# Kernel tuning notes

Measured on AMD Instinct MI355X. Metric: run time of the kernel, lower is better.

The kernel has to match this reference:

```python
import jax, jax.numpy as jnp
import numpy as np

D_MODEL = 1024
N_HEADS = 16
D_KV = D_MODEL // N_HEADS
MAX_SEQ = 2048
THETA = 10000.0
BATCH = 2
SEQ = 2048


def setup_inputs() -> dict:
    key = jax.random.key(0)
    ks = jax.random.split(key, 5)
    std = np.sqrt(2.0 / (D_MODEL + D_MODEL))
    x = jax.random.normal(ks[0], (BATCH, SEQ, D_MODEL), dtype=jnp.float32)
    wq = jax.random.normal(ks[1], (D_MODEL, D_MODEL), dtype=jnp.float32) * std
    wk = jax.random.normal(ks[2], (D_MODEL, D_MODEL), dtype=jnp.float32) * std
    wv = jax.random.normal(ks[3], (D_MODEL, D_MODEL), dtype=jnp.float32) * std
    wo = jax.random.normal(ks[4], (D_MODEL, D_MODEL), dtype=jnp.float32) * std
    token_positions = jnp.arange(SEQ, dtype=jnp.int32)
    return {"x": x, "wq": wq, "wk": wk, "wv": wv, "wo": wo,
            "token_positions": token_positions}


def _rope_tables():
    freq_range = jnp.arange(D_KV // 2, dtype=jnp.float32)
    freq = 1.0 / (THETA ** (2.0 * freq_range / D_KV))
    pos = jnp.arange(MAX_SEQ, dtype=jnp.float32)
    angs = pos[:, None] * freq[None, :]  # [max_seq, d_kv/2]
    return jnp.cos(angs), jnp.sin(angs)


def _apply_rope(xh, token_positions, cos_t, sin_t):
    # xh: [b, h, s, d_kv]
    cos_f = jnp.repeat(cos_t[token_positions], 2, axis=-1)  # [s, d_kv]
    sin_f = jnp.repeat(sin_t[token_positions], 2, axis=-1)
    pairs = xh.reshape(*xh.shape[:-1], D_KV // 2, 2)
    even, odd = pairs[..., 0], pairs[..., 1]
    rot = jnp.stack([-odd, even], axis=-1).reshape(xh.shape)
    return xh * cos_f + rot * sin_f


def reference(x, wq, wk, wv, wo, token_positions):
    b, s, _ = x.shape
    def heads(y):
        return y.reshape(b, s, N_HEADS, D_KV).transpose(0, 2, 1, 3)  # [b,h,s,d]
    q = heads(jnp.einsum('bsi,oi->bso', x, wq))
    k = heads(jnp.einsum('bsi,oi->bso', x, wk))
    v = heads(jnp.einsum('bsi,oi->bso', x, wv))
    cos_t, sin_t = _rope_tables()
    q = _apply_rope(q, token_positions, cos_t, sin_t)
    k = _apply_rope(k, token_positions, cos_t, sin_t)
    scale = 1.0 / jnp.sqrt(jnp.asarray(D_KV, x.dtype))
    scores = jnp.einsum('bhqd,bhkd->bhqk', q, k) * scale
    causal = jnp.tril(jnp.ones((s, s), dtype=bool))
    scores = jnp.where(causal, scores, -jnp.inf)
    probs = jax.nn.softmax(scores, axis=-1)
    attn = jnp.einsum('bhqk,bhkd->bhqd', probs, v)
    attn = attn.transpose(0, 2, 1, 3).reshape(b, s, D_MODEL)
    return jnp.einsum('bsi,oi->bso', attn, wo)
```

## Files before the change

kernel.cpp:

```cpp
#include <hip/hip_runtime.h>
#include <hip/hip_bf16.h>
#include <math.h>

#define SEQ 2048
#define DM 1024
#define NH 16
#define DKV 64
#define MTOT 4096
#define PSTR 40

typedef __attribute__((ext_vector_type(8))) short bf16x8;
typedef __attribute__((ext_vector_type(4))) short s16x4;
typedef __attribute__((ext_vector_type(4))) float f32x4;
typedef unsigned short ushort_t;

__device__ __forceinline__ short f2bf(float f) {
    union { float f; unsigned u; } v; v.f = f;
    unsigned r = v.u + 0x7fffu + ((v.u >> 16) & 1u);
    return (short)(r >> 16);
}

__device__ __forceinline__ bf16x8 cvt8(f32x4 a, f32x4 b) {
    union { __hip_bfloat162 h[4]; bf16x8 v; } u;
    u.h[0] = __float22bfloat162_rn(float2{a[0], a[1]});
    u.h[1] = __float22bfloat162_rn(float2{a[2], a[3]});
    u.h[2] = __float22bfloat162_rn(float2{b[0], b[1]});
    u.h[3] = __float22bfloat162_rn(float2{b[2], b[3]});
    return u.v;
}

__device__ __forceinline__ s16x4 cvt4(float a, float b, float c, float d) {
    union { __hip_bfloat162 h[2]; s16x4 v; } u;
    u.h[0] = __float22bfloat162_rn(float2{a, b});
    u.h[1] = __float22bfloat162_rn(float2{c, d});
    return u.v;
}

__device__ __forceinline__ void gload_lds16(const void* g, void* l) {
    __builtin_amdgcn_global_load_lds(
        (const __attribute__((address_space(1))) unsigned int*)g,
        (__attribute__((address_space(3))) unsigned int*)l, 16, 0, 0);
}

__global__ void cvt_kernel(const float* __restrict__ wq, const float* __restrict__ wk,
                           const float* __restrict__ wv, ushort_t* __restrict__ Wqkv) {
    int tid = blockIdx.x * blockDim.x + threadIdx.x;
    int z = tid >> 17;
    int off = (tid & 131071) * 8;
    const float* src = (z == 0) ? wq : (z == 1) ? wk : wv;
    f32x4 a = ((const f32x4*)(src + off))[0];
    f32x4 b = ((const f32x4*)(src + off))[1];
    *(bf16x8*)&Wqkv[(size_t)z * 1048576 + off] = cvt8(a, b);
}

__global__ void cvt_x_kernel(const float* __restrict__ x, ushort_t* __restrict__ xb) {
    int tid = blockIdx.x * blockDim.x + threadIdx.x;
    int off = tid * 8;
    f32x4 a = ((const f32x4*)(x + off))[0];
    f32x4 b = ((const f32x4*)(x + off))[1];
    *(bf16x8*)&xb[off] = cvt8(a, b);
}

__global__ void rope_table_kernel(float* __restrict__ cos_t, float* __restrict__ sin_t) {
    int tid = blockIdx.x * blockDim.x + threadIdx.x;
    int i = tid & 31, pos = tid >> 5;
    double freq = pow(10000.0, -(double)(2 * i) / 64.0);
    double ang = (double)pos * freq;
    cos_t[tid] = (float)cos(ang);
    sin_t[tid] = (float)sin(ang);
}

__global__ __launch_bounds__(256) void proj_qkv_kernel(
    const ushort_t* __restrict__ xb, const ushort_t* __restrict__ Wqkv,
    const float* __restrict__ cos_t, const float* __restrict__ sin_t,
    const int* __restrict__ tokpos,
    ushort_t* __restrict__ Qg, ushort_t* __restrict__ Kg, ushort_t* __restrict__ Vt)
{
    __shared__ __align__(16) short lA[2][128 * 32];
    __shared__ __align__(16) short lB[2][128 * 32];

    const int t = threadIdx.x;
    const int lane = t & 63;
    const int wid = t >> 6;
    const int quad = lane >> 4, l16 = lane & 15;
    const int mh = wid >> 1, nh = wid & 1;
    const int Mb = blockIdx.y * 128;
    const int NbG = blockIdx.x * 128;
    const int z = NbG >> 10;
    const int Nb = NbG & 1023;

    f32x4 acc[4][4] = {};

    auto stage = [&](int buf, int k0) {
        #pragma unroll
        for (int i = 0; i < 2; ++i) {
            int rbase = wid * 32 + i * 16;
            int row = rbase + (lane >> 2);
            int gch = (lane & 3) ^ ((lane >> 3) & 3);
            gload_lds16(xb + (size_t)(Mb + row) * DM + k0 + gch * 8, &lA[buf][rbase * 32]);
        }
        #pragma unroll
        for (int i = 0; i < 2; ++i) {
            int rbase = wid * 32 + i * 16;
            int row = rbase + (lane >> 2);
            int gch = (lane & 3) ^ ((lane >> 3) & 3);
            gload_lds16(Wqkv + (size_t)(NbG + row) * DM + k0 + gch * 8, &lB[buf][rbase * 32]);
        }
    };

    stage(0, 0);

    for (int kt = 0; kt < 32; ++kt) {
        const int cur = kt & 1;
        __syncthreads();
        if (kt < 31) stage(cur ^ 1, kt * 32 + 32);

        bf16x8 a[4], b[4];
        #pragma unroll
        for (int mt = 0; mt < 4; ++mt) {
            int row = mh * 64 + mt * 16 + l16;
            int slot = quad ^ ((l16 >> 1) & 3);
            a[mt] = *(const bf16x8*)&lA[cur][row * 32 + slot * 8];
        }
        #pragma unroll
        for (int nt = 0; nt < 4; ++nt) {
            int row = nh * 64 + nt * 16 + l16;
            int slot = quad ^ ((l16 >> 1) & 3);
            b[nt] = *(const bf16x8*)&lB[cur][row * 32 + slot * 8];
        }
        #pragma unroll
        for (int mt = 0; mt < 4; ++mt)
            #pragma unroll
            for (int nt = 0; nt < 4; ++nt)
                acc[mt][nt] = __builtin_amdgcn_mfma_f32_16x16x32_bf16(a[mt], b[nt], acc[mt][nt], 0, 0, 0);
    }

    const int bb = Mb >> 11;
    if (z == 2) {
        #pragma unroll
        for (int mt = 0; mt < 4; ++mt) {
            const int s0 = (Mb + mh * 64 + mt * 16 + quad * 4) & (SEQ - 1);
            #pragma unroll
            for (int nt = 0; nt < 4; ++nt) {
                int col = Nb + nh * 64 + nt * 16 + l16;
                int h = col >> 6, d = col & 63;
                s16x4 pk;
                #pragma unroll
                for (int r = 0; r < 4; ++r) pk[r] = f2bf(acc[mt][nt][r]);
                *(s16x4*)&Vt[((size_t)(bb * NH + h) * DKV + d) * SEQ + s0] = pk;
            }
        }
    } else {
        ushort_t* dst = (z == 0) ? Qg : Kg;
        #pragma unroll
        for (int mt = 0; mt < 4; ++mt) {
            #pragma unroll
            for (int nt = 0; nt < 4; ++nt) {
                #pragma unroll
                for (int r = 0; r < 4; ++r) {
                    int row = Mb + mh * 64 + mt * 16 + quad * 4 + r;
                    int s = row & (SEQ - 1);
                    int col = Nb + nh * 64 + nt * 16 + l16;
                    int h = col >> 6, d = col & 63;
                    float val = acc[mt][nt][r];
                    float part = __shfl_xor(val, 1, 64);
                    int pos = tokpos[s];
                    int i = d >> 1;
                    float c = cos_t[pos * 32 + i];
                    float sn = sin_t[pos * 32 + i];
                    val = (d & 1) ? (val * c + part * sn) : (val * c - part * sn);
                    dst[((size_t)(bb * NH + h) * SEQ + s) * DKV + d] = (ushort_t)f2bf(val);
                }
            }
        }
    }
}

__global__ __launch_bounds__(128, 4) void attn_kernel(
    const ushort_t* __restrict__ Q, const ushort_t* __restrict__ K,
    const ushort_t* __restrict__ Vt, ushort_t* __restrict__ O)
{
    __shared__ __align__(16) short lK[2][32 * 64];
    __shared__ __align__(16) short lV[2][64 * 32];
    __shared__ __align__(16) short lP[2][32 * PSTR];

    const int t = threadIdx.x;
    const int lane = t & 63;
    const int wid = t >> 6;
    const int quad = lane >> 4, l16 = lane & 15;
    const int bh = blockIdx.y;
    const int qt = gridDim.x - 1 - blockIdx.x;
    const int q0 = qt * 64;
    const int q0w = q0 + wid * 32;
    const int nkt = 2 * qt + 2;

    const ushort_t* Qb = Q + (size_t)bh * SEQ * DKV;
    const ushort_t* Kb = K + (size_t)bh * SEQ * DKV;
    const ushort_t* Vtb = Vt + (size_t)bh * DKV * SEQ;

    auto stage = [&](int kb, int buf) {
        #pragma unroll
        for (int j = 0; j < 2; ++j) {
            int rbase = wid * 16 + j * 8;
            int row = rbase + (lane >> 3);
            int gch = (lane & 7) ^ (row & 7);
            gload_lds16(Kb + (size_t)(kb + row) * DKV + gch * 8, &lK[buf][rbase * 64]);
        }
        #pragma unroll
        for (int j = 0; j < 2; ++j) {
            int rbase = wid * 32 + j * 16;
            int row = rbase + (lane >> 2);
            int gch = (lane & 3) ^ ((lane >> 3) & 3);
            gload_lds16(Vtb + (size_t)row * SEQ + kb + gch * 8, &lV[buf][rbase * 32]);
        }
    };

    bf16x8 bq[2][2];
    #pragma unroll
    for (int nt = 0; nt < 2; ++nt)
        #pragma unroll
        for (int h = 0; h < 2; ++h)
            bq[nt][h] = *(const bf16x8*)(Qb + (size_t)(q0w + nt * 16 + l16) * DKV + h * 32 + quad * 8);

    f32x4 acc[2][4] = {};
    float ps[2] = {0.f, 0.f};
    short* myP = lP[wid];

    stage(0, 0);

    for (int kt = 0; kt < nkt; ++kt) {
        const int kbase = kt * 32;
        __syncthreads();
        if (kt + 1 < nkt) stage(kbase + 32, (kt + 1) & 1);

        const short* bK = lK[kt & 1];
        const short* bV = lV[kt & 1];

        bf16x8 ak[2][2];
        #pragma unroll
        for (int mt = 0; mt < 2; ++mt)
            #pragma unroll
            for (int h = 0; h < 2; ++h) {
                int row = mt * 16 + l16;
                int slot = (h * 4 + quad) ^ (row & 7);
                ak[mt][h] = *(const bf16x8*)&bK[row * 64 + slot * 8];
            }

        f32x4 st[2][2];
        #pragma unroll
        for (int mt = 0; mt < 2; ++mt)
            #pragma unroll
            for (int nt = 0; nt < 2; ++nt) {
                f32x4 zz = {};
                zz = __builtin_amdgcn_mfma_f32_16x16x32_bf16(ak[mt][0], bq[nt][0], zz, 0, 0, 0);
                zz = __builtin_amdgcn_mfma_f32_16x16x32_bf16(ak[mt][1], bq[nt][1], zz, 0, 0, 0);
                st[mt][nt] = zz;
            }

        if (kbase >= q0w) {
            #pragma unroll
            for (int mt = 0; mt < 2; ++mt)
                #pragma unroll
                for (int nt = 0; nt < 2; ++nt) {
                    float pv[4];
                    #pragma unroll
                    for (int r = 0; r < 4; ++r) {
                        int k_abs = kbase + mt * 16 + quad * 4 + r;
                        int q_abs = q0w + nt * 16 + l16;
                        pv[r] = (k_abs > q_abs) ? 0.f : __expf(st[mt][nt][r] * 0.125f);
                        ps[nt] += pv[r];
                    }
                    *(s16x4*)&myP[(nt * 16 + l16) * PSTR + mt * 16 + quad * 4] =
                        cvt4(pv[0], pv[1], pv[2], pv[3]);
                }
        } else {
            #pragma unroll
            for (int mt = 0; mt < 2; ++mt)
                #pragma unroll
                for (int nt = 0; nt < 2; ++nt) {
                    float pv[4];
                    #pragma unroll
                    for (int r = 0; r < 4; ++r) {
                        pv[r] = __expf(st[mt][nt][r] * 0.125f);
                        ps[nt] += pv[r];
                    }
                    *(s16x4*)&myP[(nt * 16 + l16) * PSTR + mt * 16 + quad * 4] =
                        cvt4(pv[0], pv[1], pv[2], pv[3]);
                }
        }

        bf16x8 ap[2];
        #pragma unroll
        for (int mg = 0; mg < 2; ++mg)
            ap[mg] = *(const bf16x8*)&myP[(mg * 16 + l16) * PSTR + quad * 8];

        #pragma unroll
        for (int d = 0; d < 4; ++d) {
            int row = d * 16 + l16;
            int slot = quad ^ ((l16 >> 1) & 3);
            bf16x8 bv = *(const bf16x8*)&bV[row * 32 + slot * 8];
            #pragma unroll
            for (int mg = 0; mg < 2; ++mg)
                acc[mg][d] = __builtin_amdgcn_mfma_f32_16x16x32_bf16(ap[mg], bv, acc[mg][d], 0, 0, 0);
        }
    }

    #pragma unroll
    for (int g = 0; g < 2; ++g) {
        float v = ps[g];
        v += __shfl_xor(v, 16, 64);
        v += __shfl_xor(v, 32, 64);
        ps[g] = v;
    }
    float* lLw = (float*)myP;
    if (quad == 0) { lLw[l16] = ps[0]; lLw[16 + l16] = ps[1]; }
    const int bb = bh >> 4, h = bh & 15;
    #pragma unroll
    for (int mg = 0; mg < 2; ++mg) {
        f32x4 lv = *(const f32x4*)&lLw[mg * 16 + quad * 4];
        f32x4 inv;
        #pragma unroll
        for (int r = 0; r < 4; ++r) inv[r] = 1.0f / lv[r];
        #pragma unroll
        for (int d = 0; d < 4; ++d)
            #pragma unroll
            for (int r = 0; r < 4; ++r) {
                int qrow = q0w + mg * 16 + quad * 4 + r;
                int dd = d * 16 + l16;
                O[(size_t)(bb * SEQ + qrow) * DM + h * DKV + dd] = (ushort_t)f2bf(acc[mg][d][r] * inv[r]);
            }
    }
}

__global__ __launch_bounds__(256) void oproj_kernel(
    const ushort_t* __restrict__ A, const float* __restrict__ w, float* __restrict__ out)
{
    __shared__ __align__(16) short lA[2][64 * 32];
    __shared__ __align__(16) float lBf[2][128 * 32];

    const int t = threadIdx.x;
    const int lane = t & 63;
    const int wid = t >> 6;
    const int quad = lane >> 4, l16 = lane & 15;
    const int mh = wid >> 1, nh = wid & 1;
    const int Mb = blockIdx.y * 64;
    const int Nb = blockIdx.x * 128;

    f32x4 acc[2][4] = {};

    auto stage = [&](int buf, int k0) {
        {
            int rbase = wid * 16;
            int row = rbase + (lane >> 2);
            int gch = (lane & 3) ^ ((lane >> 3) & 3);
            gload_lds16(A + (size_t)(Mb + row) * DM + k0 + gch * 8, &lA[buf][rbase * 32]);
        }
        #pragma unroll
        for (int i = 0; i < 4; ++i) {
            int rbase = wid * 32 + i * 8;
            int row = rbase + (lane >> 3);
            int gch = (lane & 7) ^ (row & 7);
            gload_lds16(w + (size_t)(Nb + row) * DM + k0 + gch * 4, &lBf[buf][rbase * 32]);
        }
    };

    stage(0, 0);

    for (int kt = 0; kt < 32; ++kt) {
        const int cur = kt & 1;
        __syncthreads();
        if (kt < 31) stage(cur ^ 1, kt * 32 + 32);

        bf16x8 a[2], b[4];
        #pragma unroll
        for (int mt = 0; mt < 2; ++mt) {
            int row = mh * 32 + mt * 16 + l16;
            int slot = quad ^ ((l16 >> 1) & 3);
            a[mt] = *(const bf16x8*)&lA[cur][row * 32 + slot * 8];
        }
        #pragma unroll
        for (int nt = 0; nt < 4; ++nt) {
            int row = nh * 64 + nt * 16 + l16;
            int p0 = (2 * quad) ^ (row & 7);
            int p1 = (2 * quad + 1) ^ (row & 7);
            f32x4 q0 = *(const f32x4*)&lBf[cur][row * 32 + p0 * 4];
            f32x4 q1 = *(const f32x4*)&lBf[cur][row * 32 + p1 * 4];
            b[nt] = cvt8(q0, q1);
        }
        #pragma unroll
        for (int mt = 0; mt < 2; ++mt)
            #pragma unroll
            for (int nt = 0; nt < 4; ++nt)
                acc[mt][nt] = __builtin_amdgcn_mfma_f32_16x16x32_bf16(a[mt], b[nt], acc[mt][nt], 0, 0, 0);
    }

    #pragma unroll
    for (int mt = 0; mt < 2; ++mt)
        #pragma unroll
        for (int nt = 0; nt < 4; ++nt)
            #pragma unroll
            for (int r = 0; r < 4; ++r) {
                int row = Mb + mh * 32 + mt * 16 + quad * 4 + r;
                int col = Nb + nh * 64 + nt * 16 + l16;
                out[(size_t)row * DM + col] = acc[mt][nt][r];
            }
}

extern "C" void kernel_launch(void* const* d_in, const int* in_sizes, int n_in,
                              void* d_out, int out_size, void* d_ws, size_t ws_size,
                              hipStream_t stream) {
    const float* x  = (const float*)d_in[0];
    const float* wq = (const float*)d_in[1];
    const float* wk = (const float*)d_in[2];
    const float* wv = (const float*)d_in[3];
    const float* wo = (const float*)d_in[4];
    const int* tokpos = (const int*)d_in[5];
    float* out = (float*)d_out;

    char* ws = (char*)d_ws;
    float* cos_t    = (float*)ws;
    float* sin_t    = (float*)(ws + 256 * 1024);
    ushort_t* Wqkv  = (ushort_t*)(ws + 512 * 1024);
    ushort_t* AO    = (ushort_t*)ws;
    ushort_t* Qg    = (ushort_t*)(ws + (size_t)8  * 1024 * 1024);
    ushort_t* Kg    = (ushort_t*)(ws + (size_t)16 * 1024 * 1024);
    ushort_t* Vt    = (ushort_t*)(ws + (size_t)24 * 1024 * 1024);
    ushort_t* xb    = (ushort_t*)d_out;

    cvt_kernel<<<1536, 256, 0, stream>>>(wq, wk, wv, Wqkv);
    cvt_x_kernel<<<2048, 256, 0, stream>>>(x, xb);
    rope_table_kernel<<<256, 256, 0, stream>>>(cos_t, sin_t);
    proj_qkv_kernel<<<dim3(3 * DM / 128, MTOT / 128), 256, 0, stream>>>(
        xb, Wqkv, cos_t, sin_t, tokpos, Qg, Kg, Vt);
    attn_kernel<<<dim3(SEQ / 64, 32), 128, 0, stream>>>(Qg, Kg, Vt, AO);
    oproj_kernel<<<dim3(DM / 128, MTOT / 64), 256, 0, stream>>>(AO, wo, out);
}
```

Baseline: 240.1 us.

## Shrink attention query tile to 32 rows per block with 16 per wave

Each attention block now handles 32 query rows (16 per wave) instead of 64, doubling the grid and raising the occupancy hint to 8 blocks per CU. The causal loop runs qt+1 key tiles per block, and each K/V tile loaded into LDS is reused by half as many query rows. This lowers per-thread registers and improves load balance and parallelism, at the cost of more K/V traffic per query and less MFMA work per LDS load.

```diff
diff --git a/kernel.cpp b/kernel.cpp
--- a/kernel.cpp
+++ b/kernel.cpp
@@ -176,13 +176,13 @@
     }
 }
 
-__global__ __launch_bounds__(128, 4) void attn_kernel(
+__global__ __launch_bounds__(128, 8) void attn_kernel(
     const ushort_t* __restrict__ Q, const ushort_t* __restrict__ K,
     const ushort_t* __restrict__ Vt, ushort_t* __restrict__ O)
 {
     __shared__ __align__(16) short lK[2][32 * 64];
     __shared__ __align__(16) short lV[2][64 * 32];
-    __shared__ __align__(16) short lP[2][32 * PSTR];
+    __shared__ __align__(16) short lP[2][16 * PSTR];
 
     const int t = threadIdx.x;
     const int lane = t & 63;
@@ -190,9 +190,9 @@
     const int quad = lane >> 4, l16 = lane & 15;
     const int bh = blockIdx.y;
     const int qt = gridDim.x - 1 - blockIdx.x;
-    const int q0 = qt * 64;
-    const int q0w = q0 + wid * 32;
-    const int nkt = 2 * qt + 2;
+    const int q0 = qt * 32;
+    const int q0w = q0 + wid * 16;
+    const int nkt = qt + 1;
 
     const ushort_t* Qb = Q + (size_t)bh * SEQ * DKV;
     const ushort_t* Kb = K + (size_t)bh * SEQ * DKV;
@@ -215,15 +215,13 @@
         }
     };
 
-    bf16x8 bq[2][2];
+    bf16x8 bq[2];
     #pragma unroll
-    for (int nt = 0; nt < 2; ++nt)
-        #pragma unroll
-        for (int h = 0; h < 2; ++h)
-            bq[nt][h] = *(const bf16x8*)(Qb + (size_t)(q0w + nt * 16 + l16) * DKV + h * 32 + quad * 8);
-
-    f32x4 acc[2][4] = {};
-    float ps[2] = {0.f, 0.f};
+    for (int h = 0; h < 2; ++h)
+        bq[h] = *(const bf16x8*)(Qb + (size_t)(q0w + l16) * DKV + h * 32 + quad * 8);
+
+    f32x4 acc[4] = {};
+    float ps = 0.f;
     short* myP = lP[wid];
 
     stage(0, 0);
@@ -246,90 +244,69 @@
                 ak[mt][h] = *(const bf16x8*)&bK[row * 64 + slot * 8];
             }
 
-        f32x4 st[2][2];
-        #pragma unroll
-        for (int mt = 0; mt < 2; ++mt)
-            #pragma unroll
-            for (int nt = 0; nt < 2; ++nt) {
-                f32x4 zz = {};
-                zz = __builtin_amdgcn_mfma_f32_16x16x32_bf16(ak[mt][0], bq[nt][0], zz, 0, 0, 0);
-                zz = __builtin_amdgcn_mfma_f32_16x16x32_bf16(ak[mt][1], bq[nt][1], zz, 0, 0, 0);
-                st[mt][nt] = zz;
-            }
-
-        if (kbase >= q0w) {
-            #pragma unroll
-            for (int mt = 0; mt < 2; ++mt)
+        f32x4 st[2];
+        #pragma unroll
+        for (int mt = 0; mt < 2; ++mt) {
+            f32x4 zz = {};
+            zz = __builtin_amdgcn_mfma_f32_16x16x32_bf16(ak[mt][0], bq[0], zz, 0, 0, 0);
+            zz = __builtin_amdgcn_mfma_f32_16x16x32_bf16(ak[mt][1], bq[1], zz, 0, 0, 0);
+            st[mt] = zz;
+        }
+
+        if (kbase + 31 > q0w) {
+            #pragma unroll
+            for (int mt = 0; mt < 2; ++mt) {
+                float pv[4];
                 #pragma unroll
-                for (int nt = 0; nt < 2; ++nt) {
-                    float pv[4];
-                    #pragma unroll
-                    for (int r = 0; r < 4; ++r) {
-                        int k_abs = kbase + mt * 16 + quad * 4 + r;
-                        int q_abs = q0w + nt * 16 + l16;
-                        pv[r] = (k_abs > q_abs) ? 0.f : __expf(st[mt][nt][r] * 0.125f);
-                        ps[nt] += pv[r];
-                    }
-                    *(s16x4*)&myP[(nt * 16 + l16) * PSTR + mt * 16 + quad * 4] =
-                        cvt4(pv[0], pv[1], pv[2], pv[3]);
+                for (int r = 0; r < 4; ++r) {
+                    int k_abs = kbase + mt * 16 + quad * 4 + r;
+                    int q_abs = q0w + l16;
+                    pv[r] = (k_abs > q_abs) ? 0.f : __expf(st[mt][r] * 0.125f);
+                    ps += pv[r];
                 }
+                *(s16x4*)&myP[l16 * PSTR + mt * 16 + quad * 4] = cvt4(pv[0], pv[1], pv[2], pv[3]);
+            }
         } else {
             #pragma unroll
-            for (int mt = 0; mt < 2; ++mt)
+            for (int mt = 0; mt < 2; ++mt) {
+                float pv[4];
                 #pragma unroll
-                for (int nt = 0; nt < 2; ++nt) {
-                    float pv[4];
-                    #pragma unroll
-                    for (int r = 0; r < 4; ++r) {
-                        pv[r] = __expf(st[mt][nt][r] * 0.125f);
-                        ps[nt] += pv[r];
-                    }
-                    *(s16x4*)&myP[(nt * 16 + l16) * PSTR + mt * 16 + quad * 4] =
-                        cvt4(pv[0], pv[1], pv[2], pv[3]);
+                for (int r = 0; r < 4; ++r) {
+                    pv[r] = __expf(st[mt][r] * 0.125f);
+                    ps += pv[r];
                 }
-        }
-
-        bf16x8 ap[2];
-        #pragma unroll
-        for (int mg = 0; mg < 2; ++mg)
-            ap[mg] = *(const bf16x8*)&myP[(mg * 16 + l16) * PSTR + quad * 8];
+                *(s16x4*)&myP[l16 * PSTR + mt * 16 + quad * 4] = cvt4(pv[0], pv[1], pv[2], pv[3]);
+            }
+        }
+
+        bf16x8 ap = *(const bf16x8*)&myP[l16 * PSTR + quad * 8];
 
         #pragma unroll
         for (int d = 0; d < 4; ++d) {
             int row = d * 16 + l16;
             int slot = quad ^ ((l16 >> 1) & 3);
             bf16x8 bv = *(const bf16x8*)&bV[row * 32 + slot * 8];
-            #pragma unroll
-            for (int mg = 0; mg < 2; ++mg)
-                acc[mg][d] = __builtin_amdgcn_mfma_f32_16x16x32_bf16(ap[mg], bv, acc[mg][d], 0, 0, 0);
+            acc[d] = __builtin_amdgcn_mfma_f32_16x16x32_bf16(ap, bv, acc[d], 0, 0, 0);
         }
     }
 
+    ps += __shfl_xor(ps, 16, 64);
+    ps += __shfl_xor(ps, 32, 64);
+    float* lLw = (float*)myP;
+    if (quad == 0) lLw[l16] = ps;
+    const int bb = bh >> 4, h = bh & 15;
+    f32x4 lv = *(const f32x4*)&lLw[quad * 4];
+    f32x4 inv;
     #pragma unroll
-    for (int g = 0; g < 2; ++g) {
-        float v = ps[g];
-        v += __shfl_xor(v, 16, 64);
-        v += __shfl_xor(v, 32, 64);
-        ps[g] = v;
-    }
-    float* lLw = (float*)myP;
-    if (quad == 0) { lLw[l16] = ps[0]; lLw[16 + l16] = ps[1]; }
-    const int bb = bh >> 4, h = bh & 15;
+    for (int r = 0; r < 4; ++r) inv[r] = 1.0f / lv[r];
     #pragma unroll
-    for (int mg = 0; mg < 2; ++mg) {
-        f32x4 lv = *(const f32x4*)&lLw[mg * 16 + quad * 4];
-        f32x4 inv;
-        #pragma unroll
-        for (int r = 0; r < 4; ++r) inv[r] = 1.0f / lv[r];
-        #pragma unroll
-        for (int d = 0; d < 4; ++d)
-            #pragma unroll
-            for (int r = 0; r < 4; ++r) {
-                int qrow = q0w + mg * 16 + quad * 4 + r;
-                int dd = d * 16 + l16;
-                O[(size_t)(bb * SEQ + qrow) * DM + h * DKV + dd] = (ushort_t)f2bf(acc[mg][d][r] * inv[r]);
-            }
-    }
+    for (int d = 0; d < 4; ++d)
+        #pragma unroll
+        for (int r = 0; r < 4; ++r) {
+            int qrow = q0w + quad * 4 + r;
+            int dd = d * 16 + l16;
+            O[(size_t)(bb * SEQ + qrow) * DM + h * DKV + dd] = (ushort_t)f2bf(acc[d][r] * inv[r]);
+        }
 }
 
 __global__ __launch_bounds__(256) void oproj_kernel(
@@ -432,6 +409,6 @@
     rope_table_kernel<<<256, 256, 0, stream>>>(cos_t, sin_t);
     proj_qkv_kernel<<<dim3(3 * DM / 128, MTOT / 128), 256, 0, stream>>>(
         xb, Wqkv, cos_t, sin_t, tokpos, Qg, Kg, Vt);
-    attn_kernel<<<dim3(SEQ / 64, 32), 128, 0, stream>>>(Qg, Kg, Vt, AO);
+    attn_kernel<<<dim3(SEQ / 32, 32), 128, 0, stream>>>(Qg, Kg, Vt, AO);
     oproj_kernel<<<dim3(DM / 128, MTOT / 64), 256, 0, stream>>>(AO, wo, out);
 }
```

New measurement: 244.4 us. Within noise of the previous version (+1.8%).
